# Performance work log

Hardware: AMD Instinct MI355X
Metric: run time of the kernel (lower is better)

Reference implementation:

```python
import jax, jax.numpy as jnp
import numpy as np

N_NODES = 30000
N_EDGES = 150000
N_REL = 10
IN_DIM = 256
OUT_DIM = 256


def setup_inputs() -> dict:
    key = jax.random.key(0)
    ks = jax.random.split(key, 10)
    s = 1.0 / np.sqrt(IN_DIM)  # ~nn.Linear init scale
    return {
        "x": jax.random.normal(ks[0], (N_NODES, IN_DIM), jnp.float32),
        "W_self": jax.random.uniform(ks[1], (IN_DIM, OUT_DIM), jnp.float32, -s, s),
        "b_self": jax.random.uniform(ks[2], (OUT_DIM,), jnp.float32, -s, s),
        "W_fwd": jax.random.uniform(ks[3], (N_REL, IN_DIM, OUT_DIM), jnp.float32, -s, s),
        "b_fwd": jax.random.uniform(ks[4], (N_REL, OUT_DIM), jnp.float32, -s, s),
        "W_rev": jax.random.uniform(ks[5], (N_REL, IN_DIM, OUT_DIM), jnp.float32, -s, s),
        "b_rev": jax.random.uniform(ks[6], (N_REL, OUT_DIM), jnp.float32, -s, s),
        "dep_idx": jax.random.randint(ks[7], (N_EDGES,), 0, N_NODES, jnp.int32),
        "rel_idx": jax.random.randint(ks[8], (N_EDGES,), 0, N_REL, jnp.int32),
        "gov_idx": jax.random.randint(ks[9], (N_EDGES,), 0, N_NODES, jnp.int32),
    }


def reference(x, W_self, b_self, W_fwd, b_fwd, W_rev, b_rev, dep_idx, rel_idx, gov_idx):
    # self transform for every token: [N, out]
    out = x @ W_self + b_self
    # transform all nodes by every relation weight up-front: [R, N, out]
    H_fwd = jnp.einsum("ni,rio->rno", x, W_fwd) + b_fwd[:, None, :]
    H_rev = jnp.einsum("ni,rio->rno", x, W_rev) + b_rev[:, None, :]
    # per-edge gather: forward msg uses governor feature, reverse msg uses dependent
    msg_fwd = H_fwd[rel_idx, gov_idx]  # [E, out]
    msg_rev = H_rev[rel_idx, dep_idx]  # [E, out]
    # scatter-add: forward msg -> dependent, reverse msg -> governor
    out = out.at[dep_idx].add(msg_fwd)
    out = out.at[gov_idx].add(msg_rev)
    return out
```

## Files before the change

kernel.cpp:

```cpp
#include <hip/hip_runtime.h>

#define N_NODES 30000
#define N_EDGES 150000
#define N_REL 10
#define DIM 256

#define SORT_BLOCKS 120
#define SORT_CHUNK ((N_EDGES + SORT_BLOCKS - 1) / SORT_BLOCKS)

#define SCAN_CHUNK 256
#define SCAN_BLOCKS ((N_NODES + SCAN_CHUNK - 1) / SCAN_CHUNK)

#define A_STRIDE 280

typedef __attribute__((ext_vector_type(8))) short bf16x8;
typedef __attribute__((ext_vector_type(4))) float f32x4;

__device__ __forceinline__ unsigned short f2bf(float f) {
  union { float f; unsigned int u; } v; v.f = f;
  unsigned int u = v.u;
  unsigned int r = u + 0x7fffu + ((u >> 16) & 1u);
  return (unsigned short)(r >> 16);
}


__global__ void conv_x_kernel(const float* __restrict__ x,
                              unsigned short* __restrict__ xbf) {
  int idx = blockIdx.x * blockDim.x + threadIdx.x;
  float4 v = reinterpret_cast<const float4*>(x)[idx];
  ushort4 o;
  o.x = f2bf(v.x); o.y = f2bf(v.y); o.z = f2bf(v.z); o.w = f2bf(v.w);
  reinterpret_cast<ushort4*>(xbf)[idx] = o;
}

__global__ void conv_w_kernel(const float* __restrict__ Wf,
                              const float* __restrict__ Wr,
                              const float* __restrict__ Ws,
                              unsigned short* __restrict__ wt) {
  int idx = blockIdx.x * blockDim.x + threadIdx.x;
  int b = idx >> 16;
  int t = idx & 65535;
  int o = t >> 8, i = t & 255;
  const float* src = (b < N_REL) ? (Wf + (size_t)b * 65536)
                   : (b < 2 * N_REL) ? (Wr + (size_t)(b - N_REL) * 65536)
                   : Ws;
  wt[idx] = f2bf(src[i * 256 + o]);
}


__global__ void blockhist_kernel(const int* __restrict__ rel,
                                 int* __restrict__ block_counts) {
  __shared__ int h[N_REL];
  if (threadIdx.x < N_REL) h[threadIdx.x] = 0;
  __syncthreads();
  int beg = blockIdx.x * SORT_CHUNK;
  int end = min(beg + SORT_CHUNK, N_EDGES);
  for (int e = beg + threadIdx.x; e < end; e += blockDim.x)
    atomicAdd(&h[rel[e]], 1);
  __syncthreads();
  if (threadIdx.x < N_REL)
    block_counts[blockIdx.x * N_REL + threadIdx.x] = h[threadIdx.x];
}

__global__ void scan_rel_kernel(const int* __restrict__ block_counts,
                                int* __restrict__ rel_start,
                                int* __restrict__ block_offset) {
  __shared__ int tot[N_REL];
  int r = threadIdx.x;
  if (r < N_REL) {
    int s = 0;
    for (int b = 0; b < SORT_BLOCKS; ++b) s += block_counts[b * N_REL + r];
    tot[r] = s;
  }
  __syncthreads();
  if (threadIdx.x == 0) {
    int s = 0;
    for (int i = 0; i < N_REL; ++i) { rel_start[i] = s; s += tot[i]; }
    rel_start[N_REL] = s;
  }
  __syncthreads();
  if (r < N_REL) {
    int run = rel_start[r];
    for (int b = 0; b < SORT_BLOCKS; ++b) {
      block_offset[b * N_REL + r] = run;
      run += block_counts[b * N_REL + r];
    }
  }
}

__global__ void scatter2_kernel(const int* __restrict__ rel,
                                const int* __restrict__ block_offset,
                                int* __restrict__ perm) {
  __shared__ int cur[N_REL];
  if (threadIdx.x < N_REL)
    cur[threadIdx.x] = block_offset[blockIdx.x * N_REL + threadIdx.x];
  __syncthreads();
  int beg = blockIdx.x * SORT_CHUNK;
  int end = min(beg + SORT_CHUNK, N_EDGES);
  for (int e = beg + threadIdx.x; e < end; e += blockDim.x) {
    int pos = atomicAdd(&cur[rel[e]], 1);
    perm[pos] = e;
  }
}


__global__ void zero_cnt_kernel(int* __restrict__ cnt, int n) {
  int i = blockIdx.x * blockDim.x + threadIdx.x;
  if (i < n) cnt[i] = 0;
}

__global__ void hist_dst_kernel(const int* __restrict__ dep,
                                const int* __restrict__ gov,
                                int* __restrict__ cnt) {
  int e = blockIdx.x * blockDim.x + threadIdx.x;
  if (e < N_EDGES) {
    atomicAdd(&cnt[dep[e]], 1);
    atomicAdd(&cnt[N_NODES + gov[e]], 1);
  }
}

__global__ void scanA_kernel(const int* __restrict__ cnt,
                             int* __restrict__ tmp, int* __restrict__ sums) {
  __shared__ int s[SCAN_CHUNK];
  int d = blockIdx.y, b = blockIdx.x, t = threadIdx.x;
  int i = b * SCAN_CHUNK + t;
  int v = (i < N_NODES) ? cnt[d * N_NODES + i] : 0;
  s[t] = v;
  __syncthreads();
  for (int off = 1; off < SCAN_CHUNK; off <<= 1) {
    int add = (t >= off) ? s[t - off] : 0;
    __syncthreads();
    s[t] += add;
    __syncthreads();
  }
  if (i < N_NODES) tmp[d * N_NODES + i] = s[t] - v;
  if (t == SCAN_CHUNK - 1) sums[d * SCAN_BLOCKS + b] = s[t];
}

__global__ void scanB_kernel(const int* __restrict__ sums,
                             int* __restrict__ chunk_off, int* __restrict__ rp) {
  __shared__ int s[128];
  int d = blockIdx.x, t = threadIdx.x;
  int v = (t < SCAN_BLOCKS) ? sums[d * SCAN_BLOCKS + t] : 0;
  s[t] = v;
  __syncthreads();
  for (int off = 1; off < 128; off <<= 1) {
    int add = (t >= off) ? s[t - off] : 0;
    __syncthreads();
    s[t] += add;
    __syncthreads();
  }
  if (t < SCAN_BLOCKS) chunk_off[d * SCAN_BLOCKS + t] = s[t] - v;
  if (t == 127) rp[d * (N_NODES + 1) + N_NODES] = s[127];
}

__global__ void scanC_kernel(const int* __restrict__ tmp,
                             const int* __restrict__ chunk_off,
                             int* __restrict__ rp, int* __restrict__ cursor) {
  int d = blockIdx.y;
  int i = blockIdx.x * SCAN_CHUNK + threadIdx.x;
  if (i < N_NODES) {
    int v = tmp[d * N_NODES + i] + chunk_off[d * SCAN_BLOCKS + blockIdx.x];
    rp[d * (N_NODES + 1) + i] = v;
    cursor[d * N_NODES + i] = v;
  }
}

__global__ void colidx_kernel(const int* __restrict__ perm,
                              const int* __restrict__ dep,
                              const int* __restrict__ gov,
                              int* __restrict__ cursor,
                              int* __restrict__ colf,
                              int* __restrict__ colr) {
  int p = blockIdx.x * blockDim.x + threadIdx.x;
  if (p < N_EDGES) {
    int e = perm[p];
    colf[atomicAdd(&cursor[dep[e]], 1)] = p;
    colr[atomicAdd(&cursor[N_NODES + gov[e]], 1)] = p;
  }
}


__global__ __launch_bounds__(256, 2)
void self_gemm_kernel(const unsigned short* __restrict__ xbf,
                      const unsigned short* __restrict__ wt_self,
                      const float* __restrict__ b_self,
                      float* __restrict__ out) {
  const int tid = threadIdx.x;
  const int wave = tid >> 6, lane = tid & 63;
  const int lm = lane & 15, q = lane >> 4;
  const int nb = wave * 64;

  bf16x8 wf[8][4];
  #pragma unroll
  for (int kk = 0; kk < 8; ++kk)
    #pragma unroll
    for (int ni = 0; ni < 4; ++ni)
      wf[kk][ni] = *reinterpret_cast<const bf16x8*>(
          wt_self + (size_t)(nb + ni * 16 + lm) * DIM + kk * 32 + q * 8);

  float bias[4];
  #pragma unroll
  for (int ni = 0; ni < 4; ++ni) bias[ni] = b_self[nb + ni * 16 + lm];

  const int ntiles = (N_NODES + 63) / 64;
  for (int t = blockIdx.x; t < ntiles; t += gridDim.x) {
    const int row0 = t * 64;
    const unsigned short* xr[4];
    #pragma unroll
    for (int mi = 0; mi < 4; ++mi) {
      int r = row0 + mi * 16 + lm;
      int rc = r < N_NODES ? r : N_NODES - 1;
      xr[mi] = xbf + (size_t)rc * DIM + q * 8;
    }

    f32x4 acc[4][4];
    #pragma unroll
    for (int mi = 0; mi < 4; ++mi)
      #pragma unroll
      for (int ni = 0; ni < 4; ++ni)
        acc[mi][ni] = (f32x4){0.f, 0.f, 0.f, 0.f};

    #pragma unroll
    for (int kk = 0; kk < 8; ++kk) {
      bf16x8 a[4];
      #pragma unroll
      for (int mi = 0; mi < 4; ++mi)
        a[mi] = *reinterpret_cast<const bf16x8*>(xr[mi] + kk * 32);
      #pragma unroll
      for (int mi = 0; mi < 4; ++mi)
        #pragma unroll
        for (int ni = 0; ni < 4; ++ni)
          acc[mi][ni] = __builtin_amdgcn_mfma_f32_16x16x32_bf16(a[mi], wf[kk][ni], acc[mi][ni], 0, 0, 0);
    }

    #pragma unroll
    for (int mi = 0; mi < 4; ++mi) {
      #pragma unroll
      for (int reg = 0; reg < 4; ++reg) {
        int row = row0 + mi * 16 + q * 4 + reg;
        if (row < N_NODES) {
          #pragma unroll
          for (int ni = 0; ni < 4; ++ni)
            out[(size_t)row * DIM + nb + ni * 16 + lm] = acc[mi][ni][reg] + bias[ni];
        }
      }
    }
  }
}


__global__ __launch_bounds__(256, 2)
void edge_gemm_p1_kernel(const unsigned short* __restrict__ xbf,
                         const unsigned short* __restrict__ wt,
                         const float* __restrict__ b_fwd,
                         const float* __restrict__ b_rev,
                         const int* __restrict__ perm,
                         const int* __restrict__ rel_start,
                         const int* __restrict__ dep,
                         const int* __restrict__ gov,
                         unsigned short* __restrict__ msg) {
  const int bkt = blockIdx.y;
  const int r = bkt % N_REL;
  const bool fwd = bkt < N_REL;
  const int* src_idx = fwd ? gov : dep;
  unsigned short* mdir = msg + (fwd ? 0 : (size_t)N_EDGES * DIM);
  const int beg = rel_start[r];
  const int cnt = rel_start[r + 1] - beg;
  const int ntiles = (cnt + 63) >> 6;

  const int tid = threadIdx.x;
  const int wave = tid >> 6, lane = tid & 63;
  const int lm = lane & 15, q = lane >> 4;
  const int nb = wave * 64;

  __shared__ int s_src[64];
  __shared__ unsigned short sA[64 * A_STRIDE];

  bf16x8 wf[8][4];
  const unsigned short* wbase = wt + (size_t)bkt * DIM * DIM;
  #pragma unroll
  for (int kk = 0; kk < 8; ++kk)
    #pragma unroll
    for (int ni = 0; ni < 4; ++ni)
      wf[kk][ni] = *reinterpret_cast<const bf16x8*>(
          wbase + (size_t)(nb + ni * 16 + lm) * DIM + kk * 32 + q * 8);

  const float* bptr = (fwd ? b_fwd : b_rev) + r * DIM;
  float bias[4];
  #pragma unroll
  for (int ni = 0; ni < 4; ++ni) bias[ni] = bptr[nb + ni * 16 + lm];

  for (int t = blockIdx.x; t < ntiles; t += gridDim.x) {
    const int tile0 = t << 6;
    const int rows_valid = min(64, cnt - tile0);

    if (tid < 64) {
      int s = 0;
      if (tid < rows_valid) s = src_idx[perm[beg + tile0 + tid]];
      s_src[tid] = s;
    }
    __syncthreads();

    {
      int half = lane >> 5;
      int lcol = lane & 31;
      #pragma unroll
      for (int i = 0; i < 8; ++i) {
        int row = wave * 16 + i * 2 + half;
        uint4 v = *reinterpret_cast<const uint4*>(
            xbf + (size_t)s_src[row] * DIM + lcol * 8);
        *reinterpret_cast<uint4*>(sA + row * A_STRIDE + lcol * 8) = v;
      }
    }
    __syncthreads();

    f32x4 acc[4][4];
    #pragma unroll
    for (int mi = 0; mi < 4; ++mi)
      #pragma unroll
      for (int ni = 0; ni < 4; ++ni)
        acc[mi][ni] = (f32x4){0.f, 0.f, 0.f, 0.f};

    #pragma unroll
    for (int kk = 0; kk < 8; ++kk) {
      bf16x8 a[4];
      #pragma unroll
      for (int mi = 0; mi < 4; ++mi)
        a[mi] = *reinterpret_cast<const bf16x8*>(
            sA + (mi * 16 + lm) * A_STRIDE + kk * 32 + q * 8);
      #pragma unroll
      for (int mi = 0; mi < 4; ++mi)
        #pragma unroll
        for (int ni = 0; ni < 4; ++ni)
          acc[mi][ni] = __builtin_amdgcn_mfma_f32_16x16x32_bf16(a[mi], wf[kk][ni], acc[mi][ni], 0, 0, 0);
    }
    __syncthreads();

    #pragma unroll
    for (int mi = 0; mi < 4; ++mi)
      #pragma unroll
      for (int reg = 0; reg < 4; ++reg) {
        int row = mi * 16 + q * 4 + reg;
        #pragma unroll
        for (int ni = 0; ni < 4; ++ni)
          sA[row * DIM + nb + ni * 16 + lm] = f2bf(acc[mi][ni][reg] + bias[ni]);
      }
    __syncthreads();

    unsigned short* mbase = mdir + (size_t)(beg + tile0) * DIM;
    #pragma unroll
    for (int it = 0; it < 8; ++it) {
      int elem = it * 2048 + tid * 8;
      if ((elem >> 8) < rows_valid) {
        uint4 v = *reinterpret_cast<const uint4*>(sA + elem);
        *reinterpret_cast<uint4*>(mbase + elem) = v;
      }
    }
    __syncthreads();
  }
}


__global__ void reduce_both_kernel(const unsigned short* __restrict__ msg,
                                   const int* __restrict__ rp,
                                   const int* __restrict__ colf,
                                   const int* __restrict__ colr,
                                   float* __restrict__ out) {
  int n = blockIdx.x, t = threadIdx.x;
  int b0 = rp[n], e0 = rp[n + 1];
  int b1 = rp[(N_NODES + 1) + n], e1 = rp[(N_NODES + 1) + n + 1];
  if (e0 <= b0 && e1 <= b1) return;
  float acc = 0.f;
  for (int j = b0; j < e0; ++j) {
    int row = colf[j];
    unsigned int u = msg[(size_t)row * DIM + t];
    union { unsigned int u; float f; } c; c.u = u << 16;
    acc += c.f;
  }
  for (int j = b1; j < e1; ++j) {
    int row = colr[j];
    unsigned int u = msg[(size_t)(N_EDGES + row) * DIM + t];
    union { unsigned int u; float f; } c; c.u = u << 16;
    acc += c.f;
  }
  out[(size_t)n * DIM + t] += acc;
}


__global__ void edge_gemm_atomic_kernel(const unsigned short* __restrict__ xbf,
                                        const unsigned short* __restrict__ wt,
                                        const float* __restrict__ b_fwd,
                                        const float* __restrict__ b_rev,
                                        const int* __restrict__ perm,
                                        const int* __restrict__ rel_start,
                                        const int* __restrict__ dep,
                                        const int* __restrict__ gov,
                                        float* __restrict__ out) {
  const int bucket = blockIdx.y;
  const int r = bucket % N_REL;
  const bool fwd = bucket < N_REL;
  const int beg = rel_start[r];
  const int cnt = rel_start[r + 1] - beg;
  const int ntiles = (cnt + 63) >> 6;

  const int tid = threadIdx.x;
  const int wave = tid >> 6, lane = tid & 63;
  const int lm = lane & 15, q = lane >> 4;
  const int nb = wave * 64;

  __shared__ int s_src[64], s_dst[64];

  const unsigned short* wr[4];
  #pragma unroll
  for (int ni = 0; ni < 4; ++ni)
    wr[ni] = wt + (size_t)bucket * DIM * DIM + (size_t)(nb + ni * 16 + lm) * DIM + q * 8;

  const float* bptr = (fwd ? b_fwd : b_rev) + r * DIM;
  float bias[4];
  #pragma unroll
  for (int ni = 0; ni < 4; ++ni) bias[ni] = bptr[nb + ni * 16 + lm];

  for (int t = blockIdx.x; t < ntiles; t += gridDim.x) {
    const int tile0 = t << 6;
    const int rows_valid = min(64, cnt - tile0);

    if (tid < 64) {
      int s = 0, d = -1;
      if (tid < rows_valid) {
        int e = perm[beg + tile0 + tid];
        int gv = gov[e], dp = dep[e];
        s = fwd ? gv : dp;
        d = fwd ? dp : gv;
      }
      s_src[tid] = s;
      s_dst[tid] = d;
    }
    __syncthreads();

    const unsigned short* xr[4];
    #pragma unroll
    for (int mi = 0; mi < 4; ++mi)
      xr[mi] = xbf + (size_t)s_src[mi * 16 + lm] * DIM + q * 8;

    f32x4 acc[4][4];
    #pragma unroll
    for (int mi = 0; mi < 4; ++mi)
      #pragma unroll
      for (int ni = 0; ni < 4; ++ni)
        acc[mi][ni] = (f32x4){0.f, 0.f, 0.f, 0.f};

    #pragma unroll
    for (int k0 = 0; k0 < DIM; k0 += 32) {
      bf16x8 a[4], b[4];
      #pragma unroll
      for (int mi = 0; mi < 4; ++mi) a[mi] = *reinterpret_cast<const bf16x8*>(xr[mi] + k0);
      #pragma unroll
      for (int ni = 0; ni < 4; ++ni) b[ni] = *reinterpret_cast<const bf16x8*>(wr[ni] + k0);
      #pragma unroll
      for (int mi = 0; mi < 4; ++mi)
        #pragma unroll
        for (int ni = 0; ni < 4; ++ni)
          acc[mi][ni] = __builtin_amdgcn_mfma_f32_16x16x32_bf16(a[mi], b[ni], acc[mi][ni], 0, 0, 0);
    }

    #pragma unroll
    for (int mi = 0; mi < 4; ++mi) {
      #pragma unroll
      for (int reg = 0; reg < 4; ++reg) {
        int row = mi * 16 + q * 4 + reg;
        if (row < rows_valid) {
          int dst = s_dst[row];
          float* op = out + (size_t)dst * DIM + nb + lm;
          #pragma unroll
          for (int ni = 0; ni < 4; ++ni)
            atomicAdd(op + ni * 16, acc[mi][ni][reg] + bias[ni]);
        }
      }
    }
    __syncthreads();
  }
}


extern "C" void kernel_launch(void* const* d_in, const int* in_sizes, int n_in,
                              void* d_out, int out_size, void* d_ws, size_t ws_size,
                              hipStream_t stream) {
  const float* x      = (const float*)d_in[0];
  const float* W_self = (const float*)d_in[1];
  const float* b_self = (const float*)d_in[2];
  const float* W_fwd  = (const float*)d_in[3];
  const float* b_fwd  = (const float*)d_in[4];
  const float* W_rev  = (const float*)d_in[5];
  const float* b_rev  = (const float*)d_in[6];
  const int* dep = (const int*)d_in[7];
  const int* rel = (const int*)d_in[8];
  const int* gov = (const int*)d_in[9];
  float* out = (float*)d_out;

  char* base = (char*)d_ws;
  size_t off = 0;
  auto alloc = [&](size_t bytes) -> char* {
    char* p = base + off;
    off = (off + bytes + 15) & ~(size_t)15;
    return p;
  };

  unsigned short* xbf = (unsigned short*)alloc((size_t)N_NODES * DIM * 2);
  unsigned short* wt  = (unsigned short*)alloc((size_t)21 * DIM * DIM * 2);
  int* perm          = (int*)alloc((size_t)N_EDGES * 4);
  int* rel_start     = (int*)alloc(16 * 4);
  int* block_counts  = (int*)alloc(SORT_BLOCKS * N_REL * 4);
  int* block_offset  = (int*)alloc(SORT_BLOCKS * N_REL * 4);
  int* cnt       = (int*)alloc((size_t)2 * N_NODES * 4);
  int* tmp       = (int*)alloc((size_t)2 * N_NODES * 4);
  int* sums      = (int*)alloc((size_t)2 * SCAN_BLOCKS * 4);
  int* chunk_off = (int*)alloc((size_t)2 * SCAN_BLOCKS * 4);
  int* rp        = (int*)alloc((size_t)2 * (N_NODES + 1) * 4);
  int* cursor    = (int*)alloc((size_t)2 * N_NODES * 4);
  int* colf      = (int*)alloc((size_t)N_EDGES * 4);
  int* colr      = (int*)alloc((size_t)N_EDGES * 4);
  unsigned short* msg = (unsigned short*)alloc((size_t)2 * N_EDGES * DIM * 2);
  const bool two_phase = (off <= ws_size);

  conv_x_kernel<<<N_NODES * DIM / 4 / 256, 256, 0, stream>>>(x, xbf);
  conv_w_kernel<<<21 * DIM * DIM / 256, 256, 0, stream>>>(W_fwd, W_rev, W_self, wt);
  blockhist_kernel<<<SORT_BLOCKS, 256, 0, stream>>>(rel, block_counts);
  scan_rel_kernel<<<1, 64, 0, stream>>>(block_counts, rel_start, block_offset);
  scatter2_kernel<<<SORT_BLOCKS, 256, 0, stream>>>(rel, block_offset, perm);
  self_gemm_kernel<<<120, 256, 0, stream>>>(
      xbf, wt + (size_t)20 * DIM * DIM, b_self, out);

  if (two_phase) {
    zero_cnt_kernel<<<(2 * N_NODES + 255) / 256, 256, 0, stream>>>(cnt, 2 * N_NODES);
    hist_dst_kernel<<<(N_EDGES + 255) / 256, 256, 0, stream>>>(dep, gov, cnt);
    scanA_kernel<<<dim3(SCAN_BLOCKS, 2), SCAN_CHUNK, 0, stream>>>(cnt, tmp, sums);
    scanB_kernel<<<2, 128, 0, stream>>>(sums, chunk_off, rp);
    scanC_kernel<<<dim3(SCAN_BLOCKS, 2), SCAN_CHUNK, 0, stream>>>(tmp, chunk_off, rp, cursor);
    colidx_kernel<<<(N_EDGES + 255) / 256, 256, 0, stream>>>(perm, dep, gov, cursor, colf, colr);

    edge_gemm_p1_kernel<<<dim3(48, 2 * N_REL), 256, 0, stream>>>(
        xbf, wt, b_fwd, b_rev, perm, rel_start, dep, gov, msg);
    reduce_both_kernel<<<N_NODES, 256, 0, stream>>>(msg, rp, colf, colr, out);
  } else {
    edge_gemm_atomic_kernel<<<dim3(260, 20), 256, 0, stream>>>(
        xbf, wt, b_fwd, b_rev, perm, rel_start, dep, gov, out);
  }
}
```

Baseline: 329.1 us.

## Fuse edge sort and CSR build kernels; vectorize segmented reduce across four wave groups

```diff
diff --git a/kernel.cpp b/kernel.cpp
--- a/kernel.cpp
+++ b/kernel.cpp
@@ -47,16 +47,26 @@
   wt[idx] = f2bf(src[i * 256 + o]);
 }
 
-
-__global__ void blockhist_kernel(const int* __restrict__ rel,
-                                 int* __restrict__ block_counts) {
+__global__ void zero_cnt_kernel(int* __restrict__ cnt, int n) {
+  int i = blockIdx.x * blockDim.x + threadIdx.x;
+  if (i < n) cnt[i] = 0;
+}
+
+__global__ void hist_all_kernel(const int* __restrict__ rel,
+                                const int* __restrict__ dep,
+                                const int* __restrict__ gov,
+                                int* __restrict__ block_counts,
+                                int* __restrict__ cnt) {
   __shared__ int h[N_REL];
   if (threadIdx.x < N_REL) h[threadIdx.x] = 0;
   __syncthreads();
   int beg = blockIdx.x * SORT_CHUNK;
   int end = min(beg + SORT_CHUNK, N_EDGES);
-  for (int e = beg + threadIdx.x; e < end; e += blockDim.x)
+  for (int e = beg + threadIdx.x; e < end; e += blockDim.x) {
     atomicAdd(&h[rel[e]], 1);
+    atomicAdd(&cnt[dep[e]], 1);
+    atomicAdd(&cnt[N_NODES + gov[e]], 1);
+  }
   __syncthreads();
   if (threadIdx.x < N_REL)
     block_counts[blockIdx.x * N_REL + threadIdx.x] = h[threadIdx.x];
@@ -88,37 +98,6 @@
   }
 }
 
-__global__ void scatter2_kernel(const int* __restrict__ rel,
-                                const int* __restrict__ block_offset,
-                                int* __restrict__ perm) {
-  __shared__ int cur[N_REL];
-  if (threadIdx.x < N_REL)
-    cur[threadIdx.x] = block_offset[blockIdx.x * N_REL + threadIdx.x];
-  __syncthreads();
-  int beg = blockIdx.x * SORT_CHUNK;
-  int end = min(beg + SORT_CHUNK, N_EDGES);
-  for (int e = beg + threadIdx.x; e < end; e += blockDim.x) {
-    int pos = atomicAdd(&cur[rel[e]], 1);
-    perm[pos] = e;
-  }
-}
-
-
-__global__ void zero_cnt_kernel(int* __restrict__ cnt, int n) {
-  int i = blockIdx.x * blockDim.x + threadIdx.x;
-  if (i < n) cnt[i] = 0;
-}
-
-__global__ void hist_dst_kernel(const int* __restrict__ dep,
-                                const int* __restrict__ gov,
-                                int* __restrict__ cnt) {
-  int e = blockIdx.x * blockDim.x + threadIdx.x;
-  if (e < N_EDGES) {
-    atomicAdd(&cnt[dep[e]], 1);
-    atomicAdd(&cnt[N_NODES + gov[e]], 1);
-  }
-}
-
 __global__ void scanA_kernel(const int* __restrict__ cnt,
                              int* __restrict__ tmp, int* __restrict__ sums) {
   __shared__ int s[SCAN_CHUNK];
@@ -166,17 +145,25 @@
   }
 }
 
-__global__ void colidx_kernel(const int* __restrict__ perm,
-                              const int* __restrict__ dep,
-                              const int* __restrict__ gov,
-                              int* __restrict__ cursor,
-                              int* __restrict__ colf,
-                              int* __restrict__ colr) {
-  int p = blockIdx.x * blockDim.x + threadIdx.x;
-  if (p < N_EDGES) {
-    int e = perm[p];
-    colf[atomicAdd(&cursor[dep[e]], 1)] = p;
-    colr[atomicAdd(&cursor[N_NODES + gov[e]], 1)] = p;
+__global__ void scatter_all_kernel(const int* __restrict__ rel,
+                                   const int* __restrict__ dep,
+                                   const int* __restrict__ gov,
+                                   const int* __restrict__ block_offset,
+                                   int* __restrict__ cursor,
+                                   int* __restrict__ perm,
+                                   int* __restrict__ colf,
+                                   int* __restrict__ colr) {
+  __shared__ int cur[N_REL];
+  if (threadIdx.x < N_REL)
+    cur[threadIdx.x] = block_offset[blockIdx.x * N_REL + threadIdx.x];
+  __syncthreads();
+  int beg = blockIdx.x * SORT_CHUNK;
+  int end = min(beg + SORT_CHUNK, N_EDGES);
+  for (int e = beg + threadIdx.x; e < end; e += blockDim.x) {
+    int pos = atomicAdd(&cur[rel[e]], 1);
+    perm[pos] = e;
+    colf[atomicAdd(&cursor[dep[e]], 1)] = pos;
+    colr[atomicAdd(&cursor[N_NODES + gov[e]], 1)] = pos;
   }
 }
 
@@ -367,24 +354,41 @@
                                    const int* __restrict__ colf,
                                    const int* __restrict__ colr,
                                    float* __restrict__ out) {
-  int n = blockIdx.x, t = threadIdx.x;
-  int b0 = rp[n], e0 = rp[n + 1];
-  int b1 = rp[(N_NODES + 1) + n], e1 = rp[(N_NODES + 1) + n + 1];
+  const int n = blockIdx.x, t = threadIdx.x;
+  const int g = t >> 6, lane = t & 63;
+  const int b0 = rp[n], e0 = rp[n + 1];
+  const int b1 = rp[(N_NODES + 1) + n], e1 = rp[(N_NODES + 1) + n + 1];
   if (e0 <= b0 && e1 <= b1) return;
-  float acc = 0.f;
-  for (int j = b0; j < e0; ++j) {
+
+  float a0 = 0.f, a1 = 0.f, a2 = 0.f, a3 = 0.f;
+  for (int j = b0 + g; j < e0; j += 4) {
     int row = colf[j];
-    unsigned int u = msg[(size_t)row * DIM + t];
-    union { unsigned int u; float f; } c; c.u = u << 16;
-    acc += c.f;
-  }
-  for (int j = b1; j < e1; ++j) {
+    uint2 v = *reinterpret_cast<const uint2*>(msg + (size_t)row * DIM + lane * 4);
+    union { unsigned int u; float f; } c;
+    c.u = v.x << 16;          a0 += c.f;
+    c.u = v.x & 0xffff0000u;  a1 += c.f;
+    c.u = v.y << 16;          a2 += c.f;
+    c.u = v.y & 0xffff0000u;  a3 += c.f;
+  }
+  for (int j = b1 + g; j < e1; j += 4) {
     int row = colr[j];
-    unsigned int u = msg[(size_t)(N_EDGES + row) * DIM + t];
-    union { unsigned int u; float f; } c; c.u = u << 16;
-    acc += c.f;
-  }
-  out[(size_t)n * DIM + t] += acc;
+    uint2 v = *reinterpret_cast<const uint2*>(
+        msg + (size_t)(N_EDGES + row) * DIM + lane * 4);
+    union { unsigned int u; float f; } c;
+    c.u = v.x << 16;          a0 += c.f;
+    c.u = v.x & 0xffff0000u;  a1 += c.f;
+    c.u = v.y << 16;          a2 += c.f;
+    c.u = v.y & 0xffff0000u;  a3 += c.f;
+  }
+
+  __shared__ float part[4][DIM];
+  part[g][lane * 4 + 0] = a0;
+  part[g][lane * 4 + 1] = a1;
+  part[g][lane * 4 + 2] = a2;
+  part[g][lane * 4 + 3] = a3;
+  __syncthreads();
+  float s = part[0][t] + part[1][t] + part[2][t] + part[3][t];
+  out[(size_t)n * DIM + t] += s;
 }
 
 
@@ -525,24 +529,34 @@
 
   conv_x_kernel<<<N_NODES * DIM / 4 / 256, 256, 0, stream>>>(x, xbf);
   conv_w_kernel<<<21 * DIM * DIM / 256, 256, 0, stream>>>(W_fwd, W_rev, W_self, wt);
-  blockhist_kernel<<<SORT_BLOCKS, 256, 0, stream>>>(rel, block_counts);
-  scan_rel_kernel<<<1, 64, 0, stream>>>(block_counts, rel_start, block_offset);
-  scatter2_kernel<<<SORT_BLOCKS, 256, 0, stream>>>(rel, block_offset, perm);
-  self_gemm_kernel<<<120, 256, 0, stream>>>(
-      xbf, wt + (size_t)20 * DIM * DIM, b_self, out);
 
   if (two_phase) {
     zero_cnt_kernel<<<(2 * N_NODES + 255) / 256, 256, 0, stream>>>(cnt, 2 * N_NODES);
-    hist_dst_kernel<<<(N_EDGES + 255) / 256, 256, 0, stream>>>(dep, gov, cnt);
+    hist_all_kernel<<<SORT_BLOCKS, 256, 0, stream>>>(rel, dep, gov, block_counts, cnt);
+    scan_rel_kernel<<<1, 64, 0, stream>>>(block_counts, rel_start, block_offset);
     scanA_kernel<<<dim3(SCAN_BLOCKS, 2), SCAN_CHUNK, 0, stream>>>(cnt, tmp, sums);
     scanB_kernel<<<2, 128, 0, stream>>>(sums, chunk_off, rp);
     scanC_kernel<<<dim3(SCAN_BLOCKS, 2), SCAN_CHUNK, 0, stream>>>(tmp, chunk_off, rp, cursor);
-    colidx_kernel<<<(N_EDGES + 255) / 256, 256, 0, stream>>>(perm, dep, gov, cursor, colf, colr);
+    scatter_all_kernel<<<SORT_BLOCKS, 256, 0, stream>>>(
+        rel, dep, gov, block_offset, cursor, perm, colf, colr);
+
+    self_gemm_kernel<<<120, 256, 0, stream>>>(
+        xbf, wt + (size_t)20 * DIM * DIM, b_self, out);
 
     edge_gemm_p1_kernel<<<dim3(48, 2 * N_REL), 256, 0, stream>>>(
         xbf, wt, b_fwd, b_rev, perm, rel_start, dep, gov, msg);
     reduce_both_kernel<<<N_NODES, 256, 0, stream>>>(msg, rp, colf, colr, out);
   } else {
+    zero_cnt_kernel<<<(2 * N_NODES + 255) / 256, 256, 0, stream>>>(cnt, 2 * N_NODES);
+    hist_all_kernel<<<SORT_BLOCKS, 256, 0, stream>>>(rel, dep, gov, block_counts, cnt);
+    scan_rel_kernel<<<1, 64, 0, stream>>>(block_counts, rel_start, block_offset);
+    scanA_kernel<<<dim3(SCAN_BLOCKS, 2), SCAN_CHUNK, 0, stream>>>(cnt, tmp, sums);
+    scanB_kernel<<<2, 128, 0, stream>>>(sums, chunk_off, rp);
+    scanC_kernel<<<dim3(SCAN_BLOCKS, 2), SCAN_CHUNK, 0, stream>>>(tmp, chunk_off, rp, cursor);
+    scatter_all_kernel<<<SORT_BLOCKS, 256, 0, stream>>>(
+        rel, dep, gov, block_offset, cursor, perm, colf, colr);
+    self_gemm_kernel<<<120, 256, 0, stream>>>(
+        xbf, wt + (size_t)20 * DIM * DIM, b_self, out);
     edge_gemm_atomic_kernel<<<dim3(260, 20), 256, 0, stream>>>(
         xbf, wt, b_fwd, b_rev, perm, rel_start, dep, gov, out);
   }
```

New measurement: 303.0 us. 7.9% less time.
